# Performance work log

Hardware: AMD Instinct MI355X
Metric: run time of the kernel (lower is better)

Reference implementation:

```python
import jax, jax.numpy as jnp
import numpy as np

B, S, DIN, DOUT = 4, 2048, 4096, 11008

def setup_inputs() -> dict:
    key = jax.random.key(0)
    k1, k2, k3 = jax.random.split(key, 3)
    x = jax.random.normal(k1, (B, S, DIN), dtype=jnp.float32)
    # int8 weight stored as int32 for portability; values in int8 range
    weight = jax.random.randint(k2, (DOUT, DIN), -127, 128, dtype=jnp.int32)
    scales = jax.random.uniform(k3, (DOUT,), dtype=jnp.float32) * 0.02 + 0.001
    return {"x": x, "weight": weight, "scales": scales}

def reference(x, weight, scales):
    # F.linear(input, weight.to(input.dtype)) * scales
    w = weight.astype(x.dtype)                      # [DOUT, DIN]
    out = jnp.einsum('bsi,oi->bso', x, w)           # [B, S, DOUT]
    return out * scales                             # per-out-channel scale
```

## Files before the change

kernel.cpp:

```cpp
#include <hip/hip_runtime.h>
#include <hip/hip_bf16.h>

#define M_DIM 8192
#define N_DIM 11008
#define K_DIM 4096

typedef __attribute__((ext_vector_type(8))) short bf16x8;
typedef __attribute__((ext_vector_type(4))) float f32x4;
typedef __attribute__((ext_vector_type(4))) int i32x4;

__device__ __forceinline__ short f2bf(float f) {
    __hip_bfloat16 h = __float2bfloat16(f);
    short s;
    __builtin_memcpy(&s, &h, sizeof(s));
    return s;
}

__device__ __forceinline__ void gload_lds16(const void* g, void* l) {
    __builtin_amdgcn_global_load_lds(
        (const __attribute__((address_space(1))) unsigned int*)g,
        (__attribute__((address_space(3))) unsigned int*)l, 16, 0, 0);
}

#define MFMAI8(A, Bv, C) __builtin_amdgcn_mfma_i32_16x16x64_i8((A), (Bv), (C), 0, 0, 0)
#define MFMA16(A, Bv, C) __builtin_amdgcn_mfma_f32_16x16x32_bf16((A), (Bv), (C), 0, 0, 0)


__global__ __launch_bounds__(256)
void quant_x_i8(const float* __restrict__ X, char* __restrict__ Xq,
                float* __restrict__ RS) {
    const int row  = blockIdx.x * 4 + (threadIdx.x >> 6);
    const int lane = threadIdx.x & 63;
    const float* xr = X + (size_t)row * K_DIM;

    float4 v[16];
    float am = 0.0f;
    #pragma unroll
    for (int c = 0; c < 16; ++c) {
        v[c] = *reinterpret_cast<const float4*>(xr + c * 256 + lane * 4);
        am = fmaxf(am, fmaxf(fmaxf(fabsf(v[c].x), fabsf(v[c].y)),
                             fmaxf(fabsf(v[c].z), fabsf(v[c].w))));
    }
    #pragma unroll
    for (int off = 1; off < 64; off <<= 1)
        am = fmaxf(am, __shfl_xor(am, off));

    const float inv = 127.0f / am;
    int* xq32 = reinterpret_cast<int*>(Xq + (size_t)row * K_DIM);
    #pragma unroll
    for (int c = 0; c < 16; ++c) {
        int c0 = __float2int_rn(v[c].x * inv);
        int c1 = __float2int_rn(v[c].y * inv);
        int c2 = __float2int_rn(v[c].z * inv);
        int c3 = __float2int_rn(v[c].w * inv);
        xq32[c * 64 + lane] = (c0 & 255) | ((c1 & 255) << 8) |
                              ((c2 & 255) << 16) | (c3 << 24);
    }
    if (lane == 0) RS[row] = am / 127.0f;
}


__global__ __launch_bounds__(256)
void cvt_w_i8(const int* __restrict__ W, char* __restrict__ Wq, int n16) {
    int i = blockIdx.x * blockDim.x + threadIdx.x;
    const int stride = gridDim.x * blockDim.x;
    for (; i < n16; i += stride) {
        const int4* p = reinterpret_cast<const int4*>(W + (size_t)i * 16);
        int4 a = p[0], b = p[1], c = p[2], d = p[3];
        int4 o;
        o.x = (a.x & 255) | ((a.y & 255) << 8) | ((a.z & 255) << 16) | (a.w << 24);
        o.y = (b.x & 255) | ((b.y & 255) << 8) | ((b.z & 255) << 16) | (b.w << 24);
        o.z = (c.x & 255) | ((c.y & 255) << 8) | ((c.z & 255) << 16) | (c.w << 24);
        o.w = (d.x & 255) | ((d.y & 255) << 8) | ((d.z & 255) << 16) | (d.w << 24);
        *reinterpret_cast<int4*>(Wq + (size_t)i * 16) = o;
    }
}


#define STA(T, B, H) \
    gload_lds16(gA + (size_t)((H) * 128) * K_DIM + (T) * 128, \
                As + (B) * 32768 + (H) * 16384 + aw)

#define STB(T, B, H) \
    gload_lds16(gB + (size_t)((H) * 128) * K_DIM + (T) * 128, \
                Bs + (B) * 32768 + (H) * 16384 + aw)

#define TILE_BODY(T, B, MODE) do { \
    const char* Ab_ = As + (B) * 32768; \
    const char* Bb_ = Bs + (B) * 32768; \
    i32x4 a0_[4], b0_[4], a1_[4], b1_[4]; \
     \
    _Pragma("unroll") for (int m = 0; m < 4; ++m) \
        a0_[m] = *(const i32x4*)(Ab_ + fa + m * 2048 + cs0); \
    _Pragma("unroll") for (int n = 0; n < 4; ++n) \
        b0_[n] = *(const i32x4*)(Bb_ + fb + n * 2048 + cs0); \
    if ((MODE) < 2) STA((T) + 1, 1 - (B), 0); \
    __builtin_amdgcn_s_barrier(); \
    asm volatile("s_waitcnt lgkmcnt(0)" ::: "memory"); \
    __builtin_amdgcn_s_setprio(1); \
    _Pragma("unroll") for (int m = 0; m < 4; ++m) \
    _Pragma("unroll") for (int n = 0; n < 4; ++n) \
        acc[m][n] = MFMAI8(a0_[m], b0_[n], acc[m][n]); \
    __builtin_amdgcn_s_setprio(0); \
    __builtin_amdgcn_s_barrier(); \
     \
    _Pragma("unroll") for (int m = 0; m < 4; ++m) \
        a1_[m] = *(const i32x4*)(Ab_ + fa + m * 2048 + cs1); \
    _Pragma("unroll") for (int n = 0; n < 4; ++n) \
        b1_[n] = *(const i32x4*)(Bb_ + fb + n * 2048 + cs1); \
    if ((MODE) < 2) STA((T) + 1, 1 - (B), 1); \
    __builtin_amdgcn_s_barrier(); \
    asm volatile("s_waitcnt lgkmcnt(0)" ::: "memory"); \
    __builtin_amdgcn_s_setprio(1); \
    _Pragma("unroll") for (int m = 0; m < 2; ++m) \
    _Pragma("unroll") for (int n = 0; n < 4; ++n) \
        acc[m][n] = MFMAI8(a1_[m], b1_[n], acc[m][n]); \
    __builtin_amdgcn_s_setprio(0); \
    __builtin_amdgcn_s_barrier(); \
     \
    if ((MODE) == 0) { STB((T) + 2, (B), 0); STB((T) + 2, (B), 1); } \
    __builtin_amdgcn_s_setprio(1); \
    _Pragma("unroll") for (int m = 2; m < 4; ++m) \
    _Pragma("unroll") for (int n = 0; n < 4; ++n) \
        acc[m][n] = MFMAI8(a1_[m], b1_[n], acc[m][n]); \
    __builtin_amdgcn_s_setprio(0); \
    if ((MODE) == 0) asm volatile("s_waitcnt vmcnt(2)" ::: "memory"); \
    if ((MODE) == 1) asm volatile("s_waitcnt vmcnt(0)" ::: "memory"); \
    if ((MODE) < 2) __builtin_amdgcn_s_barrier(); \
} while (0)

__global__ __launch_bounds__(1024, 4)
void gemm_i8_hw(const char* __restrict__ Xq, const char* __restrict__ Wq,
                const float* __restrict__ RS, const float* __restrict__ SC,
                float* __restrict__ Out)
{
    __shared__ __attribute__((aligned(16))) char smem[131072];
    char* const As = smem;
    char* const Bs = smem + 65536;

    const int tid  = threadIdx.x;
    const int lane = tid & 63;
    const int w    = tid >> 6;
    const int wr   = w >> 2;
    const int wc   = w & 3;

    const int wg  = blockIdx.x;
    const int swz = (wg & 7) * 172 + (wg >> 3);
    const int by  = swz / 43;
    const int bx  = swz - by * 43;
    const int brow = by * 256;
    const int bcol = bx * 256;

    const int lr = lane >> 3;
    const int lc = (lane & 7) ^ lr;
    const char* gA = Xq + (size_t)(brow + w * 8 + lr) * K_DIM + (lc << 4);
    const char* gB = Wq + (size_t)(bcol + w * 8 + lr) * K_DIM + (lc << 4);
    const int aw = w * 1024;

    const int fa  = (wr * 64 + (lane & 15)) * 128;
    const int fb  = (wc * 64 + (lane & 15)) * 128;
    const int cs0 = (((lane >> 4) + 0) ^ (lane & 7)) * 16;
    const int cs1 = (((lane >> 4) + 4) ^ (lane & 7)) * 16;

    i32x4 acc[4][4] = {};

    STB(0, 0, 0); STB(0, 0, 1); STA(0, 0, 0); STA(0, 0, 1);
    STB(1, 1, 0); STB(1, 1, 1);
    asm volatile("s_waitcnt vmcnt(2)" ::: "memory");
    __builtin_amdgcn_s_barrier();

    for (int t = 0; t < 30; t += 2) {
        TILE_BODY(t, 0, 0);
        TILE_BODY(t + 1, 1, 0);
    }
    TILE_BODY(30, 0, 1);
    TILE_BODY(31, 1, 2);

    const int orow0 = brow + wr * 64 + ((lane >> 4) << 2);
    const int ocol0 = bcol + wc * 64 + (lane & 15);
    f32x4 rsv[4];
    #pragma unroll
    for (int m = 0; m < 4; ++m)
        rsv[m] = *reinterpret_cast<const f32x4*>(&RS[orow0 + m * 16]);
    #pragma unroll
    for (int n = 0; n < 4; ++n) {
        const float sc = SC[ocol0 + n * 16];
        #pragma unroll
        for (int m = 0; m < 4; ++m)
            #pragma unroll
            for (int j = 0; j < 4; ++j)
                __builtin_nontemporal_store(
                    (float)acc[m][n][j] * (rsv[m][j] * sc),
                    &Out[(size_t)(orow0 + m * 16 + j) * N_DIM + (ocol0 + n * 16)]);
    }
}


__global__ __launch_bounds__(256, 2)
void wo_int8_gemm_fused(const float* __restrict__ X, const int* __restrict__ W,
                        const float* __restrict__ SC, float* __restrict__ Out)
{
    __shared__ short Asf[128 * 64];
    __shared__ short Bsf[128 * 64];

    const int tid  = threadIdx.x;
    const int lane = tid & 63;
    const int wid  = tid >> 6;
    const int wrf  = wid >> 1;
    const int wcf  = wid & 1;
    const int brow = blockIdx.y * 128;
    const int bcol = blockIdx.x * 128;
    const int srow = tid >> 3;
    const int scol = (tid & 7) << 3;
    const int arow   = wrf * 64 + (lane & 15);
    const int brow_f = wcf * 64 + (lane & 15);
    const int koff   = (lane >> 4) << 3;

    f32x4 acc[4][4] = {};

    for (int k0 = 0; k0 < K_DIM; k0 += 64) {
        __syncthreads();
        #pragma unroll
        for (int p = 0; p < 4; ++p) {
            const int r = p * 32 + srow;
            const float4* xs = reinterpret_cast<const float4*>(
                X + (size_t)(brow + r) * K_DIM + (k0 + scol));
            float4 a0 = xs[0], a1 = xs[1];
            bf16x8 v;
            v[0] = f2bf(a0.x); v[1] = f2bf(a0.y); v[2] = f2bf(a0.z); v[3] = f2bf(a0.w);
            v[4] = f2bf(a1.x); v[5] = f2bf(a1.y); v[6] = f2bf(a1.z); v[7] = f2bf(a1.w);
            *reinterpret_cast<bf16x8*>(&Asf[(r * 64 + scol) ^ ((r & 7) << 3)]) = v;
        }
        #pragma unroll
        for (int p = 0; p < 4; ++p) {
            const int r = p * 32 + srow;
            const int4* ws = reinterpret_cast<const int4*>(
                W + (size_t)(bcol + r) * K_DIM + (k0 + scol));
            int4 b0 = ws[0], b1 = ws[1];
            bf16x8 v;
            v[0] = f2bf((float)b0.x); v[1] = f2bf((float)b0.y);
            v[2] = f2bf((float)b0.z); v[3] = f2bf((float)b0.w);
            v[4] = f2bf((float)b1.x); v[5] = f2bf((float)b1.y);
            v[6] = f2bf((float)b1.z); v[7] = f2bf((float)b1.w);
            *reinterpret_cast<bf16x8*>(&Bsf[(r * 64 + scol) ^ ((r & 7) << 3)]) = v;
        }
        __syncthreads();
        #pragma unroll
        for (int ks = 0; ks < 2; ++ks) {
            const int kb = ks * 32 + koff;
            bf16x8 af[4], bfr[4];
            #pragma unroll
            for (int m = 0; m < 4; ++m) {
                const int r = arow + m * 16;
                af[m] = *reinterpret_cast<const bf16x8*>(&Asf[(r * 64 + kb) ^ ((r & 7) << 3)]);
            }
            #pragma unroll
            for (int n = 0; n < 4; ++n) {
                const int r = brow_f + n * 16;
                bfr[n] = *reinterpret_cast<const bf16x8*>(&Bsf[(r * 64 + kb) ^ ((r & 7) << 3)]);
            }
            #pragma unroll
            for (int m = 0; m < 4; ++m)
                #pragma unroll
                for (int n = 0; n < 4; ++n)
                    acc[m][n] = MFMA16(af[m], bfr[n], acc[m][n]);
        }
    }

    const int orow0 = brow + wrf * 64 + ((lane >> 4) << 2);
    const int ocol0 = bcol + wcf * 64 + (lane & 15);
    #pragma unroll
    for (int n = 0; n < 4; ++n) {
        const float sc = SC[ocol0 + n * 16];
        #pragma unroll
        for (int m = 0; m < 4; ++m)
            #pragma unroll
            for (int j = 0; j < 4; ++j)
                Out[(size_t)(orow0 + m * 16 + j) * N_DIM + (ocol0 + n * 16)]
                    = acc[m][n][j] * sc;
    }
}

extern "C" void kernel_launch(void* const* d_in, const int* in_sizes, int n_in,
                              void* d_out, int out_size, void* d_ws, size_t ws_size,
                              hipStream_t stream) {
    const float* X  = (const float*)d_in[0];
    const int*   W  = (const int*)d_in[1];
    const float* SC = (const float*)d_in[2];
    float* Out = (float*)d_out;

    const size_t xq_bytes = (size_t)M_DIM * K_DIM;
    const size_t wq_bytes = (size_t)N_DIM * K_DIM;
    const size_t rs_bytes = (size_t)M_DIM * sizeof(float);
    if (ws_size >= xq_bytes + wq_bytes + rs_bytes) {
        char*  Xq = (char*)d_ws;
        char*  Wq = (char*)d_ws + xq_bytes;
        float* RS = (float*)((char*)d_ws + xq_bytes + wq_bytes);
        quant_x_i8<<<M_DIM / 4, 256, 0, stream>>>(X, Xq, RS);
        cvt_w_i8<<<2048, 256, 0, stream>>>(W, Wq, (int)((size_t)N_DIM * K_DIM / 16));
        gemm_i8_hw<<<(M_DIM / 256) * (N_DIM / 256), 1024, 0, stream>>>(Xq, Wq, RS, SC, Out);
    } else {
        dim3 grid(N_DIM / 128, M_DIM / 128);
        wo_int8_gemm_fused<<<grid, 256, 0, stream>>>(X, W, SC, Out);
    }
}
```

Baseline: 444.4 us.

## Restructure int8 GEMM into 8 waves with 128x64 warp tiles and triple-buffered B

Replaces the 1024-thread GEMM kernel with a 512-thread version. Each wave now computes a 128x64 output tile using two accumulator sets, so each B fragment read from LDS feeds twice as many MFMAs. A is double-buffered and B is triple-buffered, with B prefetched two tiles ahead, in a 160KB LDS allocation. The previous six barriers per K tile become one per tile, which is meant to cut LDS traffic and synchronisation stalls. In exchange, register pressure rises sharply and each CU runs half as many waves to hide latency.

```diff
diff --git a/kernel.cpp b/kernel.cpp
--- a/kernel.cpp
+++ b/kernel.cpp
@@ -77,64 +77,30 @@
 }
 
 
-#define STA(T, B, H) \
-    gload_lds16(gA + (size_t)((H) * 128) * K_DIM + (T) * 128, \
-                As + (B) * 32768 + (H) * 16384 + aw)
-
-#define STB(T, B, H) \
-    gload_lds16(gB + (size_t)((H) * 128) * K_DIM + (T) * 128, \
-                Bs + (B) * 32768 + (H) * 16384 + aw)
-
-#define TILE_BODY(T, B, MODE) do { \
-    const char* Ab_ = As + (B) * 32768; \
-    const char* Bb_ = Bs + (B) * 32768; \
-    i32x4 a0_[4], b0_[4], a1_[4], b1_[4]; \
-     \
-    _Pragma("unroll") for (int m = 0; m < 4; ++m) \
-        a0_[m] = *(const i32x4*)(Ab_ + fa + m * 2048 + cs0); \
-    _Pragma("unroll") for (int n = 0; n < 4; ++n) \
-        b0_[n] = *(const i32x4*)(Bb_ + fb + n * 2048 + cs0); \
-    if ((MODE) < 2) STA((T) + 1, 1 - (B), 0); \
-    __builtin_amdgcn_s_barrier(); \
-    asm volatile("s_waitcnt lgkmcnt(0)" ::: "memory"); \
-    __builtin_amdgcn_s_setprio(1); \
-    _Pragma("unroll") for (int m = 0; m < 4; ++m) \
-    _Pragma("unroll") for (int n = 0; n < 4; ++n) \
-        acc[m][n] = MFMAI8(a0_[m], b0_[n], acc[m][n]); \
-    __builtin_amdgcn_s_setprio(0); \
-    __builtin_amdgcn_s_barrier(); \
-     \
-    _Pragma("unroll") for (int m = 0; m < 4; ++m) \
-        a1_[m] = *(const i32x4*)(Ab_ + fa + m * 2048 + cs1); \
-    _Pragma("unroll") for (int n = 0; n < 4; ++n) \
-        b1_[n] = *(const i32x4*)(Bb_ + fb + n * 2048 + cs1); \
-    if ((MODE) < 2) STA((T) + 1, 1 - (B), 1); \
-    __builtin_amdgcn_s_barrier(); \
-    asm volatile("s_waitcnt lgkmcnt(0)" ::: "memory"); \
-    __builtin_amdgcn_s_setprio(1); \
-    _Pragma("unroll") for (int m = 0; m < 2; ++m) \
-    _Pragma("unroll") for (int n = 0; n < 4; ++n) \
-        acc[m][n] = MFMAI8(a1_[m], b1_[n], acc[m][n]); \
-    __builtin_amdgcn_s_setprio(0); \
-    __builtin_amdgcn_s_barrier(); \
-     \
-    if ((MODE) == 0) { STB((T) + 2, (B), 0); STB((T) + 2, (B), 1); } \
-    __builtin_amdgcn_s_setprio(1); \
-    _Pragma("unroll") for (int m = 2; m < 4; ++m) \
-    _Pragma("unroll") for (int n = 0; n < 4; ++n) \
-        acc[m][n] = MFMAI8(a1_[m], b1_[n], acc[m][n]); \
-    __builtin_amdgcn_s_setprio(0); \
-    if ((MODE) == 0) asm volatile("s_waitcnt vmcnt(2)" ::: "memory"); \
-    if ((MODE) == 1) asm volatile("s_waitcnt vmcnt(0)" ::: "memory"); \
-    if ((MODE) < 2) __builtin_amdgcn_s_barrier(); \
+#define ST_A(T, DSTB) do { \
+    const char* s_ = gA + (size_t)(T) * 128; \
+    char* d_ = (DSTB) + aw; \
+    gload_lds16(s_,                         d_); \
+    gload_lds16(s_ + (size_t)64  * K_DIM,   d_ + 8192); \
+    gload_lds16(s_ + (size_t)128 * K_DIM,   d_ + 16384); \
+    gload_lds16(s_ + (size_t)192 * K_DIM,   d_ + 24576); \
 } while (0)
 
-__global__ __launch_bounds__(1024, 4)
-void gemm_i8_hw(const char* __restrict__ Xq, const char* __restrict__ Wq,
+#define ST_B(T, DSTB) do { \
+    const char* s_ = gB + (size_t)(T) * 128; \
+    char* d_ = (DSTB) + aw; \
+    gload_lds16(s_,                         d_); \
+    gload_lds16(s_ + (size_t)64  * K_DIM,   d_ + 8192); \
+    gload_lds16(s_ + (size_t)128 * K_DIM,   d_ + 16384); \
+    gload_lds16(s_ + (size_t)192 * K_DIM,   d_ + 24576); \
+} while (0)
+
+__global__ __launch_bounds__(512, 2)
+void gemm_i8_nb(const char* __restrict__ Xq, const char* __restrict__ Wq,
                 const float* __restrict__ RS, const float* __restrict__ SC,
                 float* __restrict__ Out)
 {
-    __shared__ __attribute__((aligned(16))) char smem[131072];
+    __shared__ __attribute__((aligned(16))) char smem[163840];
     char* const As = smem;
     char* const Bs = smem + 65536;
 
@@ -157,30 +123,71 @@
     const char* gB = Wq + (size_t)(bcol + w * 8 + lr) * K_DIM + (lc << 4);
     const int aw = w * 1024;
 
-    const int fa  = (wr * 64 + (lane & 15)) * 128;
-    const int fb  = (wc * 64 + (lane & 15)) * 128;
+    const int fa  = (wr * 128 + (lane & 15)) * 128;
+    const int fb  = (wc * 64  + (lane & 15)) * 128;
     const int cs0 = (((lane >> 4) + 0) ^ (lane & 7)) * 16;
     const int cs1 = (((lane >> 4) + 4) ^ (lane & 7)) * 16;
 
     i32x4 acc[4][4] = {};
-
-    STB(0, 0, 0); STB(0, 0, 1); STA(0, 0, 0); STA(0, 0, 1);
-    STB(1, 1, 0); STB(1, 1, 1);
-    asm volatile("s_waitcnt vmcnt(2)" ::: "memory");
+    i32x4 acc2[4][4] = {};
+
+    char* Ac = As;            char* An = As + 32768;
+    char* Bc = Bs;  char* B1 = Bs + 32768;  char* B2 = Bs + 65536;
+
+    ST_B(0, Bc); ST_A(0, Ac);
+    ST_B(1, B1);
+    asm volatile("s_waitcnt vmcnt(4)" ::: "memory");
     __builtin_amdgcn_s_barrier();
 
-    for (int t = 0; t < 30; t += 2) {
-        TILE_BODY(t, 0, 0);
-        TILE_BODY(t + 1, 1, 0);
-    }
-    TILE_BODY(30, 0, 1);
-    TILE_BODY(31, 1, 2);
-
-    const int orow0 = brow + wr * 64 + ((lane >> 4) << 2);
+    for (int t = 0; t < 32; ++t) {
+        i32x4 a_[8][2], b_[4][2];
+        #pragma unroll
+        for (int m = 0; m < 4; ++m) {
+            a_[m][0] = *(const i32x4*)(Ac + fa + m * 2048 + cs0);
+            a_[m][1] = *(const i32x4*)(Ac + fa + m * 2048 + cs1);
+        }
+        #pragma unroll
+        for (int n = 0; n < 4; ++n) {
+            b_[n][0] = *(const i32x4*)(Bc + fb + n * 2048 + cs0);
+            b_[n][1] = *(const i32x4*)(Bc + fb + n * 2048 + cs1);
+        }
+        if (t < 31) ST_A(t + 1, An);
+        if (t < 30) ST_B(t + 2, B2);
+        #pragma unroll
+        for (int m = 0; m < 4; ++m) {
+            a_[m + 4][0] = *(const i32x4*)(Ac + fa + (m + 4) * 2048 + cs0);
+            a_[m + 4][1] = *(const i32x4*)(Ac + fa + (m + 4) * 2048 + cs1);
+        }
+        __builtin_amdgcn_s_setprio(1);
+        #pragma unroll
+        for (int m = 0; m < 4; ++m)
+            #pragma unroll
+            for (int n = 0; n < 4; ++n) {
+                acc[m][n] = MFMAI8(a_[m][0], b_[n][0], acc[m][n]);
+                acc[m][n] = MFMAI8(a_[m][1], b_[n][1], acc[m][n]);
+            }
+        #pragma unroll
+        for (int m = 0; m < 4; ++m)
+            #pragma unroll
+            for (int n = 0; n < 4; ++n) {
+                acc2[m][n] = MFMAI8(a_[m + 4][0], b_[n][0], acc2[m][n]);
+                acc2[m][n] = MFMAI8(a_[m + 4][1], b_[n][1], acc2[m][n]);
+            }
+        __builtin_amdgcn_s_setprio(0);
+        if (t < 31) {
+            if (t < 30) asm volatile("s_waitcnt vmcnt(4)" ::: "memory");
+            else        asm volatile("s_waitcnt vmcnt(0)" ::: "memory");
+            __builtin_amdgcn_s_barrier();
+        }
+        char* tA = Ac; Ac = An; An = tA;
+        char* tB = Bc; Bc = B1; B1 = B2; B2 = tB;
+    }
+
+    const int orow0 = brow + wr * 128 + ((lane >> 4) << 2);
     const int ocol0 = bcol + wc * 64 + (lane & 15);
-    f32x4 rsv[4];
-    #pragma unroll
-    for (int m = 0; m < 4; ++m)
+    f32x4 rsv[8];
+    #pragma unroll
+    for (int m = 0; m < 8; ++m)
         rsv[m] = *reinterpret_cast<const f32x4*>(&RS[orow0 + m * 16]);
     #pragma unroll
     for (int n = 0; n < 4; ++n) {
@@ -188,10 +195,14 @@
         #pragma unroll
         for (int m = 0; m < 4; ++m)
             #pragma unroll
-            for (int j = 0; j < 4; ++j)
+            for (int j = 0; j < 4; ++j) {
                 __builtin_nontemporal_store(
                     (float)acc[m][n][j] * (rsv[m][j] * sc),
                     &Out[(size_t)(orow0 + m * 16 + j) * N_DIM + (ocol0 + n * 16)]);
+                __builtin_nontemporal_store(
+                    (float)acc2[m][n][j] * (rsv[m + 4][j] * sc),
+                    &Out[(size_t)(orow0 + (m + 4) * 16 + j) * N_DIM + (ocol0 + n * 16)]);
+            }
     }
 }
 
@@ -298,7 +309,7 @@
         float* RS = (float*)((char*)d_ws + xq_bytes + wq_bytes);
         quant_x_i8<<<M_DIM / 4, 256, 0, stream>>>(X, Xq, RS);
         cvt_w_i8<<<2048, 256, 0, stream>>>(W, Wq, (int)((size_t)N_DIM * K_DIM / 16));
-        gemm_i8_hw<<<(M_DIM / 256) * (N_DIM / 256), 1024, 0, stream>>>(Xq, Wq, RS, SC, Out);
+        gemm_i8_nb<<<(M_DIM / 256) * (N_DIM / 256), 512, 0, stream>>>(Xq, Wq, RS, SC, Out);
     } else {
         dim3 grid(N_DIM / 128, M_DIM / 128);
         wo_int8_gemm_fused<<<grid, 256, 0, stream>>>(X, W, SC, Out);
```

Result: slower. 453.9 us (+2.1%).
